# Optimization experiments

Measured on AMD Instinct MI355X. Metric: run time of the kernel, lower is better.

Reference implementation:

```python
import jax, jax.numpy as jnp
import numpy as np

N = 50000   # nodes
E = 800000  # edges
K = 3       # hops per TAGConv


def _row_normalize(x):
    row_sum = jnp.clip(jnp.sum(x, axis=1, keepdims=True), 1e-8, None)
    return x / row_sum


def _gcn_norm(edge_index, num_nodes):
    # PyG gcn_norm with add_self_loops=False (TAGConv default), edge_weight=1
    src, dst = edge_index[0], edge_index[1]
    deg = jax.ops.segment_sum(jnp.ones((src.shape[0],), jnp.float32), dst,
                              num_segments=num_nodes)
    deg_inv_sqrt = jnp.where(deg > 0, jnp.where(deg > 0, deg, 1.0) ** -0.5, 0.0)
    return deg_inv_sqrt[src] * deg_inv_sqrt[dst]  # [E]


def _propagate(x, src, dst, norm, num_nodes):
    # out[dst] += norm * x[src]   (sparse sym-normalized SpMM)
    return jax.ops.segment_sum(norm[:, None] * x[src], dst, num_segments=num_nodes)


def _tagconv(x, edge_index, norm, W, b):
    # W: [K+1, d_in, d_out]; out = sum_k A_hat^k x @ W_k + b
    src, dst = edge_index[0], edge_index[1]
    n = x.shape[0]
    hops = [x]
    for _ in range(W.shape[0] - 1):
        hops.append(_propagate(hops[-1], src, dst, norm, n))
    H = jnp.stack(hops)  # [K+1, N, d_in]
    return jnp.einsum('knd,kdo->no', H, W) + b


def setup_inputs() -> dict:
    key = jax.random.key(0)
    k1, k2, k3, k4 = jax.random.split(key, 4)
    x = jax.random.normal(k1, (N, 128), jnp.float32)
    edge_index = jax.random.randint(k2, (2, E), 0, N, jnp.int32)
    W1 = jax.random.normal(k3, (K + 1, 128, 16), jnp.float32) * 0.1
    b1 = jnp.zeros((16,), jnp.float32)
    W2 = jax.random.normal(k4, (K + 1, 16, 64), jnp.float32) * 0.1
    b2 = jnp.zeros((64,), jnp.float32)
    return {"x": x, "edge_index": edge_index, "W1": W1, "b1": b1,
            "W2": W2, "b2": b2}


def reference(x, edge_index, W1, b1, W2, b2):
    n = x.shape[0]
    norm = _gcn_norm(edge_index, n)
    h = _row_normalize(x)
    h = jax.nn.relu(_tagconv(h, edge_index, norm, W1, b1))
    # dropout is identity in eval mode
    return _tagconv(h, edge_index, norm, W2, b2)
```

## Files before the change

kernel.cpp:

```cpp
#include <hip/hip_runtime.h>
#include <hip/hip_bf16.h>

typedef unsigned short u16;

__device__ __forceinline__ float bf2f(u16 h) {
    return __uint_as_float(((unsigned int)h) << 16);
}
__device__ __forceinline__ u16 f2bf(float f) {
    __hip_bfloat16 h = __float2bfloat16(f);
    return *reinterpret_cast<u16*>(&h);
}

#define BKT_SHIFT 7
#define BKT_SIZE  128
#define CHUNK     2048

__global__ __launch_bounds__(256) void hist_kernel(const int* __restrict__ dst,
                                                   int* __restrict__ hist,
                                                   int E, int nbA, int nbuck) {
    __shared__ int lh[512];
    for (int j = threadIdx.x; j < nbuck; j += 256) lh[j] = 0;
    __syncthreads();
    int base = blockIdx.x * CHUNK;
    int end  = min(E, base + CHUNK);
    for (int e = base + threadIdx.x; e < end; e += 256)
        atomicAdd(&lh[dst[e] >> BKT_SHIFT], 1);
    __syncthreads();
    for (int j = threadIdx.x; j < nbuck; j += 256)
        hist[j * nbA + blockIdx.x] = lh[j];
}

__global__ __launch_bounds__(256) void scanA_kernel(const int* __restrict__ in,
                                                    int* __restrict__ outp1,
                                                    int* __restrict__ bsum, int n) {
    __shared__ int lds[256];
    int i = blockIdx.x * 256 + threadIdx.x;
    int v = (i < n) ? in[i] : 0;
    lds[threadIdx.x] = v;
    __syncthreads();
    #pragma unroll
    for (int off = 1; off < 256; off <<= 1) {
        int t = (threadIdx.x >= off) ? lds[threadIdx.x - off] : 0;
        __syncthreads();
        lds[threadIdx.x] += t;
        __syncthreads();
    }
    if (i < n) outp1[i + 1] = lds[threadIdx.x];
    if (threadIdx.x == 255) bsum[blockIdx.x] = lds[255];
}
__global__ __launch_bounds__(1024) void scanB_kernel(int* __restrict__ bsum, int nb) {
    __shared__ int lds[1024];
    int t = threadIdx.x;
    int v = (t < nb) ? bsum[t] : 0;
    lds[t] = v;
    __syncthreads();
    #pragma unroll
    for (int off = 1; off < 1024; off <<= 1) {
        int u = (t >= off) ? lds[t - off] : 0;
        __syncthreads();
        lds[t] += u;
        __syncthreads();
    }
    if (t < nb) bsum[t] = lds[t] - v;
}
__global__ __launch_bounds__(256) void scanC_kernel(int* __restrict__ outp1,
                                                    const int* __restrict__ bsum, int n) {
    int i = blockIdx.x * 256 + threadIdx.x;
    if (i < n) outp1[i + 1] += bsum[blockIdx.x];
    if (i == 0) outp1[0] = 0;
}

__global__ __launch_bounds__(256) void bucket_scatter_kernel(
    const int* __restrict__ src, const int* __restrict__ dst,
    const int* __restrict__ hofs, int2* __restrict__ bucketed,
    int E, int nbA, int nbuck)
{
    __shared__ int lbase[512];
    __shared__ int lcnt[512];
    for (int j = threadIdx.x; j < nbuck; j += 256) {
        lbase[j] = hofs[j * nbA + blockIdx.x];
        lcnt[j] = 0;
    }
    __syncthreads();
    int base = blockIdx.x * CHUNK;
    int end  = min(E, base + CHUNK);
    for (int e = base + threadIdx.x; e < end; e += 256) {
        int d = dst[e];
        int b = d >> BKT_SHIFT;
        int r = atomicAdd(&lcnt[b], 1);
        bucketed[lbase[b] + r] = make_int2(src[e], d);
    }
}

__global__ __launch_bounds__(256) void csr_finalize_kernel(
    const int2* __restrict__ bucketed, const int* __restrict__ hofs,
    int* __restrict__ rowptr, float* __restrict__ dis,
    float2* __restrict__ ecolw, int E, int nbA, int nbuck, int n)
{
    __shared__ int cnt[BKT_SIZE];
    __shared__ int run[BKT_SIZE];
    __shared__ float disl[BKT_SIZE];
    int b = blockIdx.x;
    int bstart = hofs[b * nbA];
    int bend   = (b == nbuck - 1) ? E : hofs[(b + 1) * nbA];
    for (int j = threadIdx.x; j < BKT_SIZE; j += 256) cnt[j] = 0;
    __syncthreads();
    for (int i = bstart + threadIdx.x; i < bend; i += 256)
        atomicAdd(&cnt[bucketed[i].y & (BKT_SIZE - 1)], 1);
    __syncthreads();
    if (threadIdx.x == 0) {
        int runacc = 0;
        for (int j = 0; j < BKT_SIZE; ++j) {
            int c = cnt[j];
            run[j] = runacc;
            runacc += c;
        }
    }
    __syncthreads();
    for (int j = threadIdx.x; j < BKT_SIZE; j += 256) {
        int d = b * BKT_SIZE + j;
        if (d < n) {
            rowptr[d] = bstart + run[j];
            int c = cnt[j];
            float dv = (c > 0) ? rsqrtf((float)c) : 0.0f;
            dis[d] = dv;
            disl[j] = dv;
        }
    }
    if (b == 0 && threadIdx.x == 0) rowptr[n] = E;
    __syncthreads();
    for (int i = bstart + threadIdx.x; i < bend; i += 256) {
        int2 p = bucketed[i];
        int j = p.y & (BKT_SIZE - 1);
        int r = atomicAdd(&run[j], 1);
        ecolw[bstart + r] = make_float2(__int_as_float(p.x), disl[j]);
    }
}

__global__ __launch_bounds__(256) void weight_kernel(float2* __restrict__ ecolw,
                                                     const float* __restrict__ dis, int E) {
    int e = blockIdx.x * blockDim.x + threadIdx.x;
    if (e < E) {
        float2 c = ecolw[e];
        ecolw[e].y = c.y * dis[__float_as_int(c.x)];
    }
}

__global__ __launch_bounds__(256) void gemm1_bf_kernel(
    const float* __restrict__ x, const float* __restrict__ W1,
    u16* __restrict__ zb, int n, int nstride)
{
    __shared__ float As[64 * 132];
    __shared__ float Bs[64 * 64];
    __shared__ float sums[128];
    const int t  = threadIdx.x;
    const int tx = t & 15;
    const int ty = t >> 4;
    const int c  = t & 15;
    const int g  = t >> 4;
    const int block_row = blockIdx.x * 128;

    float acc[8][4];
    #pragma unroll
    for (int i = 0; i < 8; ++i)
        #pragma unroll
        for (int j = 0; j < 4; ++j) acc[i][j] = 0.f;

    for (int kp = 0; kp < 2; ++kp) {
        #pragma unroll
        for (int i = 0; i < 8; ++i) {
            int row  = g + 16 * i;
            int grow = block_row + row;
            float v0 = 0.f, v1 = 0.f, v2 = 0.f, v3 = 0.f;
            if (grow < n) {
                const float* xp = x + (long)grow * 128 + kp * 64 + c;
                v0 = xp[0]; v1 = xp[16]; v2 = xp[32]; v3 = xp[48];
            }
            As[(c +  0) * 132 + row] = v0;
            As[(c + 16) * 132 + row] = v1;
            As[(c + 32) * 132 + row] = v2;
            As[(c + 48) * 132 + row] = v3;
            float red = (v0 + v1) + (v2 + v3);
            #pragma unroll
            for (int off = 8; off > 0; off >>= 1) red += __shfl_down(red, off, 16);
            if (c == 0) { if (kp == 0) sums[row] = red; else sums[row] += red; }
        }
        #pragma unroll
        for (int i2 = 0; i2 < 4; ++i2) {
            int kk = g + 16 * i2;
            int kglob = kp * 64 + kk;
            float4 wv = *(const float4*)(W1 + (c >> 2) * 2048 + kglob * 16 + 4 * (c & 3));
            *(float4*)(Bs + kk * 64 + 4 * c) = wv;
        }
        __syncthreads();
        #pragma unroll 4
        for (int kk = 0; kk < 64; ++kk) {
            float4 a0 = *(const float4*)(As + kk * 132 + 8 * ty);
            float4 a1 = *(const float4*)(As + kk * 132 + 8 * ty + 4);
            float4 bv = *(const float4*)(Bs + kk * 64 + 4 * tx);
            float ar[8] = {a0.x, a0.y, a0.z, a0.w, a1.x, a1.y, a1.z, a1.w};
            float br[4] = {bv.x, bv.y, bv.z, bv.w};
            #pragma unroll
            for (int i = 0; i < 8; ++i)
                #pragma unroll
                for (int j = 0; j < 4; ++j)
                    acc[i][j] += ar[i] * br[j];
        }
        __syncthreads();
    }
    int plane = tx >> 2;
    int oo4   = 4 * (tx & 3);
    #pragma unroll
    for (int i = 0; i < 8; ++i) {
        int row  = 8 * ty + i;
        int grow = block_row + row;
        if (grow < n) {
            float s = 1.0f / fmaxf(sums[row], 1e-8f);
            ushort4 o;
            o.x = f2bf(acc[i][0] * s); o.y = f2bf(acc[i][1] * s);
            o.z = f2bf(acc[i][2] * s); o.w = f2bf(acc[i][3] * s);
            *(ushort4*)(zb + (long)plane * nstride + (long)grow * 16 + oo4) = o;
        }
    }
}

__global__ __launch_bounds__(256) void spmm_csr_bf_kernel(
    const u16* __restrict__ in, const u16* __restrict__ addsrc,
    u16* __restrict__ out, const int* __restrict__ rowptr,
    const float2* __restrict__ ecolw, const float* __restrict__ b,
    int relu, int n)
{
    int t = blockIdx.x * blockDim.x + threadIdx.x;
    int r = t >> 2, q = t & 3;
    if (r >= n) return;
    int e0 = rowptr[r], e1 = rowptr[r + 1];
    float a0x=0,a0y=0,a0z=0,a0w=0, a1x=0,a1y=0,a1z=0,a1w=0;
    float a2x=0,a2y=0,a2z=0,a2w=0, a3x=0,a3y=0,a3z=0,a3w=0;
    int e = e0;
    for (; e + 4 <= e1; e += 4) {
        float2 c0 = ecolw[e], c1 = ecolw[e+1], c2 = ecolw[e+2], c3 = ecolw[e+3];
        ushort4 v0 = *((const ushort4*)(in + (long)__float_as_int(c0.x) * 16) + q);
        ushort4 v1 = *((const ushort4*)(in + (long)__float_as_int(c1.x) * 16) + q);
        ushort4 v2 = *((const ushort4*)(in + (long)__float_as_int(c2.x) * 16) + q);
        ushort4 v3 = *((const ushort4*)(in + (long)__float_as_int(c3.x) * 16) + q);
        a0x += c0.y * bf2f(v0.x); a0y += c0.y * bf2f(v0.y); a0z += c0.y * bf2f(v0.z); a0w += c0.y * bf2f(v0.w);
        a1x += c1.y * bf2f(v1.x); a1y += c1.y * bf2f(v1.y); a1z += c1.y * bf2f(v1.z); a1w += c1.y * bf2f(v1.w);
        a2x += c2.y * bf2f(v2.x); a2y += c2.y * bf2f(v2.y); a2z += c2.y * bf2f(v2.z); a2w += c2.y * bf2f(v2.w);
        a3x += c3.y * bf2f(v3.x); a3y += c3.y * bf2f(v3.y); a3z += c3.y * bf2f(v3.z); a3w += c3.y * bf2f(v3.w);
    }
    for (; e < e1; ++e) {
        float2 c0 = ecolw[e];
        ushort4 v0 = *((const ushort4*)(in + (long)__float_as_int(c0.x) * 16) + q);
        a0x += c0.y * bf2f(v0.x); a0y += c0.y * bf2f(v0.y); a0z += c0.y * bf2f(v0.z); a0w += c0.y * bf2f(v0.w);
    }
    float Ax = (a0x+a1x)+(a2x+a3x), Ay = (a0y+a1y)+(a2y+a3y);
    float Az = (a0z+a1z)+(a2z+a3z), Aw = (a0w+a1w)+(a2w+a3w);
    if (addsrc) {
        ushort4 s = *((const ushort4*)(addsrc + (long)r * 16) + q);
        Ax += bf2f(s.x); Ay += bf2f(s.y); Az += bf2f(s.z); Aw += bf2f(s.w);
    }
    if (b) {
        float4 bb = *((const float4*)b + q);
        Ax += bb.x; Ay += bb.y; Az += bb.z; Aw += bb.w;
    }
    if (relu) {
        Ax = fmaxf(Ax, 0.f); Ay = fmaxf(Ay, 0.f);
        Az = fmaxf(Az, 0.f); Aw = fmaxf(Aw, 0.f);
    }
    ushort4 o; o.x = f2bf(Ax); o.y = f2bf(Ay); o.z = f2bf(Az); o.w = f2bf(Aw);
    *((ushort4*)(out + (long)r * 16) + q) = o;
}

__global__ __launch_bounds__(256) void gemm2_bf_kernel(
    const u16* __restrict__ zb, const float* __restrict__ W2,
    const float* __restrict__ b2, float* __restrict__ out, int n, int nstride)
{
    __shared__ float As[64 * 132];
    __shared__ float Bs[64 * 64];
    const int t  = threadIdx.x;
    const int tx = t & 15;
    const int ty = t >> 4;
    const int c  = t & 15;
    const int g  = t >> 4;
    const int block_row = blockIdx.x * 128;

    float acc[8][4];
    #pragma unroll
    for (int i = 0; i < 8; ++i)
        #pragma unroll
        for (int j = 0; j < 4; ++j) acc[i][j] = 0.f;

    #pragma unroll
    for (int i = 0; i < 8; ++i) {
        int row  = g + 16 * i;
        int grow = block_row + row;
        float v0 = 0.f, v1 = 0.f, v2 = 0.f, v3 = 0.f;
        if (grow < n) {
            const u16* zp = zb + (long)grow * 16 + c;
            v0 = bf2f(zp[0]);
            v1 = bf2f(zp[(long)nstride]);
            v2 = bf2f(zp[2 * (long)nstride]);
            v3 = bf2f(zp[3 * (long)nstride]);
        }
        As[(c +  0) * 132 + row] = v0;
        As[(c + 16) * 132 + row] = v1;
        As[(c + 32) * 132 + row] = v2;
        As[(c + 48) * 132 + row] = v3;
    }
    #pragma unroll
    for (int i2 = 0; i2 < 4; ++i2) {
        int j = g + 16 * i2;
        float4 wv = *(const float4*)(W2 + j * 64 + 4 * c);
        *(float4*)(Bs + j * 64 + 4 * c) = wv;
    }
    __syncthreads();
    #pragma unroll 4
    for (int kk = 0; kk < 64; ++kk) {
        float4 a0 = *(const float4*)(As + kk * 132 + 8 * ty);
        float4 a1 = *(const float4*)(As + kk * 132 + 8 * ty + 4);
        float4 bv = *(const float4*)(Bs + kk * 64 + 4 * tx);
        float ar[8] = {a0.x, a0.y, a0.z, a0.w, a1.x, a1.y, a1.z, a1.w};
        float br[4] = {bv.x, bv.y, bv.z, bv.w};
        #pragma unroll
        for (int i = 0; i < 8; ++i)
            #pragma unroll
            for (int j = 0; j < 4; ++j)
                acc[i][j] += ar[i] * br[j];
    }
    float4 bias = *(const float4*)(b2 + 4 * tx);
    #pragma unroll
    for (int i = 0; i < 8; ++i) {
        int grow = block_row + 8 * ty + i;
        if (grow < n) {
            float4 o = make_float4(acc[i][0] + bias.x, acc[i][1] + bias.y,
                                   acc[i][2] + bias.z, acc[i][3] + bias.w);
            *(float4*)(out + (long)grow * 64 + 4 * tx) = o;
        }
    }
}

__global__ void deg_kernel(const int* __restrict__ dst, float* __restrict__ deg, int E) {
    int e = blockIdx.x * blockDim.x + threadIdx.x;
    if (e < E) atomicAdd(&deg[dst[e]], 1.0f);
}
__global__ void disf_kernel(float* __restrict__ deg, int n) {
    int i = blockIdx.x * blockDim.x + threadIdx.x;
    if (i < n) {
        float d = deg[i];
        deg[i] = (d > 0.0f) ? rsqrtf(d) : 0.0f;
    }
}
__global__ __launch_bounds__(256) void gemm1_f32_kernel(
    const float* __restrict__ x, const float* __restrict__ W1,
    float* __restrict__ z, int n, int nstride)
{
    __shared__ float As[64 * 132];
    __shared__ float Bs[64 * 64];
    __shared__ float sums[128];
    const int t  = threadIdx.x;
    const int tx = t & 15;
    const int ty = t >> 4;
    const int c  = t & 15;
    const int g  = t >> 4;
    const int block_row = blockIdx.x * 128;
    float acc[8][4];
    #pragma unroll
    for (int i = 0; i < 8; ++i)
        #pragma unroll
        for (int j = 0; j < 4; ++j) acc[i][j] = 0.f;
    for (int kp = 0; kp < 2; ++kp) {
        #pragma unroll
        for (int i = 0; i < 8; ++i) {
            int row  = g + 16 * i;
            int grow = block_row + row;
            float v0 = 0.f, v1 = 0.f, v2 = 0.f, v3 = 0.f;
            if (grow < n) {
                const float* xp = x + (long)grow * 128 + kp * 64 + c;
                v0 = xp[0]; v1 = xp[16]; v2 = xp[32]; v3 = xp[48];
            }
            As[(c +  0) * 132 + row] = v0;
            As[(c + 16) * 132 + row] = v1;
            As[(c + 32) * 132 + row] = v2;
            As[(c + 48) * 132 + row] = v3;
            float red = (v0 + v1) + (v2 + v3);
            #pragma unroll
            for (int off = 8; off > 0; off >>= 1) red += __shfl_down(red, off, 16);
            if (c == 0) { if (kp == 0) sums[row] = red; else sums[row] += red; }
        }
        #pragma unroll
        for (int i2 = 0; i2 < 4; ++i2) {
            int kk = g + 16 * i2;
            int kglob = kp * 64 + kk;
            float4 wv = *(const float4*)(W1 + (c >> 2) * 2048 + kglob * 16 + 4 * (c & 3));
            *(float4*)(Bs + kk * 64 + 4 * c) = wv;
        }
        __syncthreads();
        #pragma unroll 4
        for (int kk = 0; kk < 64; ++kk) {
            float4 a0 = *(const float4*)(As + kk * 132 + 8 * ty);
            float4 a1 = *(const float4*)(As + kk * 132 + 8 * ty + 4);
            float4 bv = *(const float4*)(Bs + kk * 64 + 4 * tx);
            float ar[8] = {a0.x, a0.y, a0.z, a0.w, a1.x, a1.y, a1.z, a1.w};
            float br[4] = {bv.x, bv.y, bv.z, bv.w};
            #pragma unroll
            for (int i = 0; i < 8; ++i)
                #pragma unroll
                for (int j = 0; j < 4; ++j)
                    acc[i][j] += ar[i] * br[j];
        }
        __syncthreads();
    }
    int plane = tx >> 2;
    int oo4   = 4 * (tx & 3);
    #pragma unroll
    for (int i = 0; i < 8; ++i) {
        int row  = 8 * ty + i;
        int grow = block_row + row;
        if (grow < n) {
            float s = 1.0f / fmaxf(sums[row], 1e-8f);
            float4 o = make_float4(acc[i][0] * s, acc[i][1] * s, acc[i][2] * s, acc[i][3] * s);
            *(float4*)(z + (long)plane * nstride + (long)grow * 16 + oo4) = o;
        }
    }
}
__global__ __launch_bounds__(256) void spmm_atomic_kernel(
    const float* __restrict__ in, float* __restrict__ out,
    const int* __restrict__ src, const int* __restrict__ dst,
    const float* __restrict__ dis, int E)
{
    int t = blockIdx.x * blockDim.x + threadIdx.x;
    int e = t >> 4, f = t & 15;
    if (e < E) {
        int s = src[e], d = dst[e];
        atomicAdd(&out[d * 16 + f], dis[s] * dis[d] * in[s * 16 + f]);
    }
}
__global__ void bias_relu_kernel(float* __restrict__ z0, const float* __restrict__ b, int total) {
    int i = blockIdx.x * blockDim.x + threadIdx.x;
    if (i < total) {
        float v = z0[i] + b[i & 15];
        z0[i] = v > 0.0f ? v : 0.0f;
    }
}
__global__ __launch_bounds__(256) void gemm2_f32_kernel(
    const float* __restrict__ z, const float* __restrict__ W2,
    const float* __restrict__ b2, float* __restrict__ out, int n, int nstride)
{
    __shared__ float As[64 * 132];
    __shared__ float Bs[64 * 64];
    const int t  = threadIdx.x;
    const int tx = t & 15;
    const int ty = t >> 4;
    const int c  = t & 15;
    const int g  = t >> 4;
    const int block_row = blockIdx.x * 128;
    float acc[8][4];
    #pragma unroll
    for (int i = 0; i < 8; ++i)
        #pragma unroll
        for (int j = 0; j < 4; ++j) acc[i][j] = 0.f;
    #pragma unroll
    for (int i = 0; i < 8; ++i) {
        int row  = g + 16 * i;
        int grow = block_row + row;
        float v0 = 0.f, v1 = 0.f, v2 = 0.f, v3 = 0.f;
        if (grow < n) {
            const float* zp = z + (long)grow * 16 + c;
            v0 = zp[0];
            v1 = zp[(long)nstride];
            v2 = zp[2 * (long)nstride];
            v3 = zp[3 * (long)nstride];
        }
        As[(c +  0) * 132 + row] = v0;
        As[(c + 16) * 132 + row] = v1;
        As[(c + 32) * 132 + row] = v2;
        As[(c + 48) * 132 + row] = v3;
    }
    #pragma unroll
    for (int i2 = 0; i2 < 4; ++i2) {
        int j = g + 16 * i2;
        float4 wv = *(const float4*)(W2 + j * 64 + 4 * c);
        *(float4*)(Bs + j * 64 + 4 * c) = wv;
    }
    __syncthreads();
    #pragma unroll 4
    for (int kk = 0; kk < 64; ++kk) {
        float4 a0 = *(const float4*)(As + kk * 132 + 8 * ty);
        float4 a1 = *(const float4*)(As + kk * 132 + 8 * ty + 4);
        float4 bv = *(const float4*)(Bs + kk * 64 + 4 * tx);
        float ar[8] = {a0.x, a0.y, a0.z, a0.w, a1.x, a1.y, a1.z, a1.w};
        float br[4] = {bv.x, bv.y, bv.z, bv.w};
        #pragma unroll
        for (int i = 0; i < 8; ++i)
            #pragma unroll
            for (int j = 0; j < 4; ++j)
                acc[i][j] += ar[i] * br[j];
    }
    float4 bias = *(const float4*)(b2 + 4 * tx);
    #pragma unroll
    for (int i = 0; i < 8; ++i) {
        int grow = block_row + 8 * ty + i;
        if (grow < n) {
            float4 o = make_float4(acc[i][0] + bias.x, acc[i][1] + bias.y,
                                   acc[i][2] + bias.z, acc[i][3] + bias.w);
            *(float4*)(out + (long)grow * 64 + 4 * tx) = o;
        }
    }
}

static inline size_t align16(size_t v) { return (v + 15) & ~(size_t)15; }

extern "C" void kernel_launch(void* const* d_in, const int* in_sizes, int n_in,
                              void* d_out, int out_size, void* d_ws, size_t ws_size,
                              hipStream_t stream) {
    const float* x   = (const float*)d_in[0];
    const int*   ei  = (const int*)d_in[1];
    const float* W1  = (const float*)d_in[2];
    const float* b1  = (const float*)d_in[3];
    const float* W2  = (const float*)d_in[4];
    const float* bb2 = (const float*)d_in[5];
    float* out = (float*)d_out;

    const int n  = in_sizes[0] / 128;
    const int E  = in_sizes[1] / 2;
    const int NS = n * 16;

    const int* srcp = ei;
    const int* dstp = ei + E;

    const int nbuck = (n + BKT_SIZE - 1) >> BKT_SHIFT;
    const int nbA   = (E + CHUNK - 1) / CHUNK;
    const int m     = nbuck * nbA;
    const int nbS   = (m + 255) / 256;

    char* wsb = (char*)d_ws;
    int*   hist   = (int*)wsb;
    int*   hofs   = (int*)(wsb + (size_t)4 * m);
    int*   bsum   = (int*)(wsb + (size_t)4 * (2 * m + 1));
    int*   rowptr = (int*)(wsb + (size_t)4 * (2 * m + 1 + 1024));
    float* dis    = (float*)(wsb + (size_t)4 * (2 * m + 1 + 1024 + n + 1));
    size_t zoffb  = align16((size_t)4 * (2 * m + 1 + 1024 + 2 * n + 1));
    u16*   zb     = (u16*)(wsb + zoffb);
    size_t bkoff  = align16(zoffb + (size_t)2 * 4 * NS);
    int2*  bucketed = (int2*)(wsb + bkoff);
    size_t ecooff = align16(bkoff + (size_t)8 * E);
    float2* ecolw = (float2*)(wsb + ecooff);
    size_t need   = ecooff + (size_t)8 * E;

    int gemm_blocks = (n + 127) / 128;

    if (ws_size >= need && nbuck <= 512 && nbS <= 256 * 1024) {
        hist_kernel<<<nbA, 256, 0, stream>>>(dstp, hist, E, nbA, nbuck);
        if (nbS <= 1024) {
            scanA_kernel<<<nbS, 256, 0, stream>>>(hist, hofs, bsum, m);
            scanB_kernel<<<1, 1024, 0, stream>>>(bsum, nbS);
            scanC_kernel<<<nbS, 256, 0, stream>>>(hofs, bsum, m);
        }
        bucket_scatter_kernel<<<nbA, 256, 0, stream>>>(srcp, dstp, hofs, bucketed, E, nbA, nbuck);
        csr_finalize_kernel<<<nbuck, 256, 0, stream>>>(bucketed, hofs, rowptr, dis, ecolw, E, nbA, nbuck, n);
        weight_kernel<<<(E + 255) / 256, 256, 0, stream>>>(ecolw, dis, E);

        gemm1_bf_kernel<<<gemm_blocks, 256, 0, stream>>>(x, W1, zb, n, NS);

        int sb = (4 * n + 255) / 256;
        spmm_csr_bf_kernel<<<sb, 256, 0, stream>>>(zb + 3 * NS, zb + 2 * NS, zb + 2 * NS, rowptr, ecolw, nullptr, 0, n);
        spmm_csr_bf_kernel<<<sb, 256, 0, stream>>>(zb + 2 * NS, zb + 1 * NS, zb + 1 * NS, rowptr, ecolw, nullptr, 0, n);
        spmm_csr_bf_kernel<<<sb, 256, 0, stream>>>(zb + 1 * NS, zb,          zb,          rowptr, ecolw, b1,      1, n);
        spmm_csr_bf_kernel<<<sb, 256, 0, stream>>>(zb,          nullptr, zb + 1 * NS, rowptr, ecolw, nullptr, 0, n);
        spmm_csr_bf_kernel<<<sb, 256, 0, stream>>>(zb + 1 * NS, nullptr, zb + 2 * NS, rowptr, ecolw, nullptr, 0, n);
        spmm_csr_bf_kernel<<<sb, 256, 0, stream>>>(zb + 2 * NS, nullptr, zb + 3 * NS, rowptr, ecolw, nullptr, 0, n);

        gemm2_bf_kernel<<<gemm_blocks, 256, 0, stream>>>(zb, W2, bb2, out, n, NS);
    } else {
        float* ws = (float*)d_ws;
        float* dis2 = ws;
        size_t z2off = ((size_t)n + 3) & ~(size_t)3;
        float* z2 = ws + z2off;
        hipMemsetAsync(dis2, 0, n * sizeof(float), stream);
        deg_kernel<<<(E + 255) / 256, 256, 0, stream>>>(dstp, dis2, E);
        disf_kernel<<<(n + 255) / 256, 256, 0, stream>>>(dis2, n);
        gemm1_f32_kernel<<<gemm_blocks, 256, 0, stream>>>(x, W1, z2, n, NS);
        int sb = (16 * E + 255) / 256;
        spmm_atomic_kernel<<<sb, 256, 0, stream>>>(z2 + 3 * NS, z2 + 2 * NS, srcp, dstp, dis2, E);
        spmm_atomic_kernel<<<sb, 256, 0, stream>>>(z2 + 2 * NS, z2 + 1 * NS, srcp, dstp, dis2, E);
        spmm_atomic_kernel<<<sb, 256, 0, stream>>>(z2 + 1 * NS, z2,          srcp, dstp, dis2, E);
        bias_relu_kernel<<<(NS + 255) / 256, 256, 0, stream>>>(z2, b1, NS);
        hipMemsetAsync(z2 + NS, 0, (size_t)3 * NS * sizeof(float), stream);
        spmm_atomic_kernel<<<sb, 256, 0, stream>>>(z2,          z2 + NS,     srcp, dstp, dis2, E);
        spmm_atomic_kernel<<<sb, 256, 0, stream>>>(z2 + NS,     z2 + 2 * NS, srcp, dstp, dis2, E);
        spmm_atomic_kernel<<<sb, 256, 0, stream>>>(z2 + 2 * NS, z2 + 3 * NS, srcp, dstp, dis2, E);
        gemm2_f32_kernel<<<gemm_blocks, 256, 0, stream>>>(z2, W2, bb2, out, n, NS);
    }
}
```

Baseline: 214.7 us.

## Replace CSR build with bucketed edges and LDS-atomic bucket SpMM

Drops the per-row CSR finalize pass. Edges are now packed into 32-bit words holding the source and the local row, bucketed by 64-row destination groups. Degrees come from a per-bucket count, and each SpMM block accumulates its 64 rows in shared memory with LDS atomics, applying the destination normalization at write-out. This removes the finalize sort and the rowptr reads, but adds shared-memory atomic contention in every SpMM and makes the float summation order nondeterministic.

Result: slower. 672.2 us (+213.1%).

```diff
diff --git a/kernel.cpp b/kernel.cpp
--- a/kernel.cpp
+++ b/kernel.cpp
@@ -2,23 +2,24 @@
 #include <hip/hip_bf16.h>
 
 typedef unsigned short u16;
+typedef unsigned int u32;
 
 __device__ __forceinline__ float bf2f(u16 h) {
-    return __uint_as_float(((unsigned int)h) << 16);
+    return __uint_as_float(((u32)h) << 16);
 }
 __device__ __forceinline__ u16 f2bf(float f) {
     __hip_bfloat16 h = __float2bfloat16(f);
     return *reinterpret_cast<u16*>(&h);
 }
 
-#define BKT_SHIFT 7
-#define BKT_SIZE  128
-#define CHUNK     2048
+#define BKT_SHIFT 6
+#define BKT_SIZE  64
+#define CHUNK     4096
 
 __global__ __launch_bounds__(256) void hist_kernel(const int* __restrict__ dst,
                                                    int* __restrict__ hist,
                                                    int E, int nbA, int nbuck) {
-    __shared__ int lh[512];
+    __shared__ int lh[1024];
     for (int j = threadIdx.x; j < nbuck; j += 256) lh[j] = 0;
     __syncthreads();
     int base = blockIdx.x * CHUNK;
@@ -72,11 +73,11 @@
 
 __global__ __launch_bounds__(256) void bucket_scatter_kernel(
     const int* __restrict__ src, const int* __restrict__ dst,
-    const int* __restrict__ hofs, int2* __restrict__ bucketed,
+    const int* __restrict__ hofs, u32* __restrict__ bucketed,
     int E, int nbA, int nbuck)
 {
-    __shared__ int lbase[512];
-    __shared__ int lcnt[512];
+    __shared__ int lbase[1024];
+    __shared__ int lcnt[1024];
     for (int j = threadIdx.x; j < nbuck; j += 256) {
         lbase[j] = hofs[j * nbA + blockIdx.x];
         lcnt[j] = 0;
@@ -88,61 +89,110 @@
         int d = dst[e];
         int b = d >> BKT_SHIFT;
         int r = atomicAdd(&lcnt[b], 1);
-        bucketed[lbase[b] + r] = make_int2(src[e], d);
-    }
-}
-
-__global__ __launch_bounds__(256) void csr_finalize_kernel(
-    const int2* __restrict__ bucketed, const int* __restrict__ hofs,
-    int* __restrict__ rowptr, float* __restrict__ dis,
-    float2* __restrict__ ecolw, int E, int nbA, int nbuck, int n)
+        bucketed[lbase[b] + r] = (u32)src[e] | ((u32)(d & (BKT_SIZE - 1)) << 20);
+    }
+}
+
+__global__ __launch_bounds__(256) void bucketdeg_kernel(
+    const u32* __restrict__ bucketed, const int* __restrict__ hofs,
+    float* __restrict__ dis, int E, int nbA, int nbuck, int n)
 {
     __shared__ int cnt[BKT_SIZE];
-    __shared__ int run[BKT_SIZE];
-    __shared__ float disl[BKT_SIZE];
-    int b = blockIdx.x;
-    int bstart = hofs[b * nbA];
-    int bend   = (b == nbuck - 1) ? E : hofs[(b + 1) * nbA];
-    for (int j = threadIdx.x; j < BKT_SIZE; j += 256) cnt[j] = 0;
-    __syncthreads();
-    for (int i = bstart + threadIdx.x; i < bend; i += 256)
-        atomicAdd(&cnt[bucketed[i].y & (BKT_SIZE - 1)], 1);
-    __syncthreads();
-    if (threadIdx.x == 0) {
-        int runacc = 0;
-        for (int j = 0; j < BKT_SIZE; ++j) {
-            int c = cnt[j];
-            run[j] = runacc;
-            runacc += c;
-        }
-    }
-    __syncthreads();
-    for (int j = threadIdx.x; j < BKT_SIZE; j += 256) {
-        int d = b * BKT_SIZE + j;
-        if (d < n) {
-            rowptr[d] = bstart + run[j];
-            int c = cnt[j];
-            float dv = (c > 0) ? rsqrtf((float)c) : 0.0f;
-            dis[d] = dv;
-            disl[j] = dv;
-        }
-    }
-    if (b == 0 && threadIdx.x == 0) rowptr[n] = E;
-    __syncthreads();
-    for (int i = bstart + threadIdx.x; i < bend; i += 256) {
-        int2 p = bucketed[i];
-        int j = p.y & (BKT_SIZE - 1);
-        int r = atomicAdd(&run[j], 1);
-        ecolw[bstart + r] = make_float2(__int_as_float(p.x), disl[j]);
-    }
-}
-
-__global__ __launch_bounds__(256) void weight_kernel(float2* __restrict__ ecolw,
-                                                     const float* __restrict__ dis, int E) {
+    int bkt = blockIdx.x;
+    if (threadIdx.x < BKT_SIZE) cnt[threadIdx.x] = 0;
+    __syncthreads();
+    int estart = hofs[bkt * nbA];
+    int eend   = (bkt + 1 < nbuck) ? hofs[(bkt + 1) * nbA] : E;
+    for (int e = estart + threadIdx.x; e < eend; e += 256)
+        atomicAdd(&cnt[bucketed[e] >> 20], 1);
+    __syncthreads();
+    if (threadIdx.x < BKT_SIZE) {
+        int r = bkt * BKT_SIZE + threadIdx.x;
+        if (r < n) {
+            int c = cnt[threadIdx.x];
+            dis[r] = (c > 0) ? rsqrtf((float)c) : 0.0f;
+        }
+    }
+}
+
+__global__ __launch_bounds__(256) void weight_kernel(const u32* __restrict__ bucketed,
+                                                     const float* __restrict__ dis,
+                                                     float2* __restrict__ ecolw, int E) {
     int e = blockIdx.x * blockDim.x + threadIdx.x;
     if (e < E) {
-        float2 c = ecolw[e];
-        ecolw[e].y = c.y * dis[__float_as_int(c.x)];
+        u32 p = bucketed[e];
+        ecolw[e] = make_float2(__int_as_float((int)p), dis[p & 0xFFFFFu]);
+    }
+}
+
+__global__ __launch_bounds__(256) void spmm_bucket_kernel(
+    const u16* __restrict__ in, const u16* __restrict__ addsrc,
+    u16* __restrict__ out, const int* __restrict__ hofs,
+    const float2* __restrict__ ecolw, const float* __restrict__ dis,
+    const float* __restrict__ b, int relu, int E, int nbA, int nbuck, int n)
+{
+    __shared__ float acc[BKT_SIZE * 16];
+    int bkt = blockIdx.x;
+    int estart = hofs[bkt * nbA];
+    int eend   = (bkt + 1 < nbuck) ? hofs[(bkt + 1) * nbA] : E;
+    #pragma unroll
+    for (int j = threadIdx.x; j < BKT_SIZE * 16; j += 256) acc[j] = 0.f;
+    __syncthreads();
+
+    int g = threadIdx.x >> 2;
+    int q = threadIdx.x & 3;
+    int e = estart + g;
+    for (; e + 64 < eend; e += 128) {
+        float2 c0 = ecolw[e];
+        float2 c1 = ecolw[e + 64];
+        u32 p0 = (u32)__float_as_int(c0.x);
+        u32 p1 = (u32)__float_as_int(c1.x);
+        ushort4 v0 = *((const ushort4*)(in + (size_t)(p0 & 0xFFFFFu) * 16) + q);
+        ushort4 v1 = *((const ushort4*)(in + (size_t)(p1 & 0xFFFFFu) * 16) + q);
+        float* a0 = acc + (p0 >> 20) * 16 + 4 * q;
+        float* a1 = acc + (p1 >> 20) * 16 + 4 * q;
+        atomicAdd(a0 + 0, c0.y * bf2f(v0.x));
+        atomicAdd(a0 + 1, c0.y * bf2f(v0.y));
+        atomicAdd(a0 + 2, c0.y * bf2f(v0.z));
+        atomicAdd(a0 + 3, c0.y * bf2f(v0.w));
+        atomicAdd(a1 + 0, c1.y * bf2f(v1.x));
+        atomicAdd(a1 + 1, c1.y * bf2f(v1.y));
+        atomicAdd(a1 + 2, c1.y * bf2f(v1.z));
+        atomicAdd(a1 + 3, c1.y * bf2f(v1.w));
+    }
+    if (e < eend) {
+        float2 c0 = ecolw[e];
+        u32 p0 = (u32)__float_as_int(c0.x);
+        ushort4 v0 = *((const ushort4*)(in + (size_t)(p0 & 0xFFFFFu) * 16) + q);
+        float* a0 = acc + (p0 >> 20) * 16 + 4 * q;
+        atomicAdd(a0 + 0, c0.y * bf2f(v0.x));
+        atomicAdd(a0 + 1, c0.y * bf2f(v0.y));
+        atomicAdd(a0 + 2, c0.y * bf2f(v0.z));
+        atomicAdd(a0 + 3, c0.y * bf2f(v0.w));
+    }
+    __syncthreads();
+
+    int row = threadIdx.x >> 2;
+    int qq  = threadIdx.x & 3;
+    int r   = bkt * BKT_SIZE + row;
+    if (r < n) {
+        float dr = dis[r];
+        const float* ap = acc + row * 16 + 4 * qq;
+        float Ax = ap[0] * dr, Ay = ap[1] * dr, Az = ap[2] * dr, Aw = ap[3] * dr;
+        if (addsrc) {
+            ushort4 s = *((const ushort4*)(addsrc + (size_t)r * 16) + qq);
+            Ax += bf2f(s.x); Ay += bf2f(s.y); Az += bf2f(s.z); Aw += bf2f(s.w);
+        }
+        if (b) {
+            float4 bb = *((const float4*)b + qq);
+            Ax += bb.x; Ay += bb.y; Az += bb.z; Aw += bb.w;
+        }
+        if (relu) {
+            Ax = fmaxf(Ax, 0.f); Ay = fmaxf(Ay, 0.f);
+            Az = fmaxf(Az, 0.f); Aw = fmaxf(Aw, 0.f);
+        }
+        ushort4 o; o.x = f2bf(Ax); o.y = f2bf(Ay); o.z = f2bf(Az); o.w = f2bf(Aw);
+        *((ushort4*)(out + (size_t)r * 16) + qq) = o;
     }
 }
 
@@ -224,53 +274,6 @@
     }
 }
 
-__global__ __launch_bounds__(256) void spmm_csr_bf_kernel(
-    const u16* __restrict__ in, const u16* __restrict__ addsrc,
-    u16* __restrict__ out, const int* __restrict__ rowptr,
-    const float2* __restrict__ ecolw, const float* __restrict__ b,
-    int relu, int n)
-{
-    int t = blockIdx.x * blockDim.x + threadIdx.x;
-    int r = t >> 2, q = t & 3;
-    if (r >= n) return;
-    int e0 = rowptr[r], e1 = rowptr[r + 1];
-    float a0x=0,a0y=0,a0z=0,a0w=0, a1x=0,a1y=0,a1z=0,a1w=0;
-    float a2x=0,a2y=0,a2z=0,a2w=0, a3x=0,a3y=0,a3z=0,a3w=0;
-    int e = e0;
-    for (; e + 4 <= e1; e += 4) {
-        float2 c0 = ecolw[e], c1 = ecolw[e+1], c2 = ecolw[e+2], c3 = ecolw[e+3];
-        ushort4 v0 = *((const ushort4*)(in + (long)__float_as_int(c0.x) * 16) + q);
-        ushort4 v1 = *((const ushort4*)(in + (long)__float_as_int(c1.x) * 16) + q);
-        ushort4 v2 = *((const ushort4*)(in + (long)__float_as_int(c2.x) * 16) + q);
-        ushort4 v3 = *((const ushort4*)(in + (long)__float_as_int(c3.x) * 16) + q);
-        a0x += c0.y * bf2f(v0.x); a0y += c0.y * bf2f(v0.y); a0z += c0.y * bf2f(v0.z); a0w += c0.y * bf2f(v0.w);
-        a1x += c1.y * bf2f(v1.x); a1y += c1.y * bf2f(v1.y); a1z += c1.y * bf2f(v1.z); a1w += c1.y * bf2f(v1.w);
-        a2x += c2.y * bf2f(v2.x); a2y += c2.y * bf2f(v2.y); a2z += c2.y * bf2f(v2.z); a2w += c2.y * bf2f(v2.w);
-        a3x += c3.y * bf2f(v3.x); a3y += c3.y * bf2f(v3.y); a3z += c3.y * bf2f(v3.z); a3w += c3.y * bf2f(v3.w);
-    }
-    for (; e < e1; ++e) {
-        float2 c0 = ecolw[e];
-        ushort4 v0 = *((const ushort4*)(in + (long)__float_as_int(c0.x) * 16) + q);
-        a0x += c0.y * bf2f(v0.x); a0y += c0.y * bf2f(v0.y); a0z += c0.y * bf2f(v0.z); a0w += c0.y * bf2f(v0.w);
-    }
-    float Ax = (a0x+a1x)+(a2x+a3x), Ay = (a0y+a1y)+(a2y+a3y);
-    float Az = (a0z+a1z)+(a2z+a3z), Aw = (a0w+a1w)+(a2w+a3w);
-    if (addsrc) {
-        ushort4 s = *((const ushort4*)(addsrc + (long)r * 16) + q);
-        Ax += bf2f(s.x); Ay += bf2f(s.y); Az += bf2f(s.z); Aw += bf2f(s.w);
-    }
-    if (b) {
-        float4 bb = *((const float4*)b + q);
-        Ax += bb.x; Ay += bb.y; Az += bb.z; Aw += bb.w;
-    }
-    if (relu) {
-        Ax = fmaxf(Ax, 0.f); Ay = fmaxf(Ay, 0.f);
-        Az = fmaxf(Az, 0.f); Aw = fmaxf(Aw, 0.f);
-    }
-    ushort4 o; o.x = f2bf(Ax); o.y = f2bf(Ay); o.z = f2bf(Az); o.w = f2bf(Aw);
-    *((ushort4*)(out + (long)r * 16) + q) = o;
-}
-
 __global__ __launch_bounds__(256) void gemm2_bf_kernel(
     const u16* __restrict__ zb, const float* __restrict__ W2,
     const float* __restrict__ b2, float* __restrict__ out, int n, int nstride)
@@ -537,38 +540,34 @@
     int*   hist   = (int*)wsb;
     int*   hofs   = (int*)(wsb + (size_t)4 * m);
     int*   bsum   = (int*)(wsb + (size_t)4 * (2 * m + 1));
-    int*   rowptr = (int*)(wsb + (size_t)4 * (2 * m + 1 + 1024));
-    float* dis    = (float*)(wsb + (size_t)4 * (2 * m + 1 + 1024 + n + 1));
-    size_t zoffb  = align16((size_t)4 * (2 * m + 1 + 1024 + 2 * n + 1));
+    float* dis    = (float*)(wsb + (size_t)4 * (2 * m + 1 + 1024));
+    size_t zoffb  = align16((size_t)4 * (2 * m + 1 + 1024 + n));
     u16*   zb     = (u16*)(wsb + zoffb);
     size_t bkoff  = align16(zoffb + (size_t)2 * 4 * NS);
-    int2*  bucketed = (int2*)(wsb + bkoff);
-    size_t ecooff = align16(bkoff + (size_t)8 * E);
+    u32*   bucketed = (u32*)(wsb + bkoff);
+    size_t ecooff = align16(bkoff + (size_t)4 * E);
     float2* ecolw = (float2*)(wsb + ecooff);
     size_t need   = ecooff + (size_t)8 * E;
 
     int gemm_blocks = (n + 127) / 128;
 
-    if (ws_size >= need && nbuck <= 512 && nbS <= 256 * 1024) {
+    if (ws_size >= need && n < (1 << 20) && nbuck <= 1024 && nbS <= 1024) {
         hist_kernel<<<nbA, 256, 0, stream>>>(dstp, hist, E, nbA, nbuck);
-        if (nbS <= 1024) {
-            scanA_kernel<<<nbS, 256, 0, stream>>>(hist, hofs, bsum, m);
-            scanB_kernel<<<1, 1024, 0, stream>>>(bsum, nbS);
-            scanC_kernel<<<nbS, 256, 0, stream>>>(hofs, bsum, m);
-        }
+        scanA_kernel<<<nbS, 256, 0, stream>>>(hist, hofs, bsum, m);
+        scanB_kernel<<<1, 1024, 0, stream>>>(bsum, nbS);
+        scanC_kernel<<<nbS, 256, 0, stream>>>(hofs, bsum, m);
         bucket_scatter_kernel<<<nbA, 256, 0, stream>>>(srcp, dstp, hofs, bucketed, E, nbA, nbuck);
-        csr_finalize_kernel<<<nbuck, 256, 0, stream>>>(bucketed, hofs, rowptr, dis, ecolw, E, nbA, nbuck, n);
-        weight_kernel<<<(E + 255) / 256, 256, 0, stream>>>(ecolw, dis, E);
+        bucketdeg_kernel<<<nbuck, 256, 0, stream>>>(bucketed, hofs, dis, E, nbA, nbuck, n);
+        weight_kernel<<<(E + 255) / 256, 256, 0, stream>>>(bucketed, dis, ecolw, E);
 
         gemm1_bf_kernel<<<gemm_blocks, 256, 0, stream>>>(x, W1, zb, n, NS);
 
-        int sb = (4 * n + 255) / 256;
-        spmm_csr_bf_kernel<<<sb, 256, 0, stream>>>(zb + 3 * NS, zb + 2 * NS, zb + 2 * NS, rowptr, ecolw, nullptr, 0, n);
-        spmm_csr_bf_kernel<<<sb, 256, 0, stream>>>(zb + 2 * NS, zb + 1 * NS, zb + 1 * NS, rowptr, ecolw, nullptr, 0, n);
-        spmm_csr_bf_kernel<<<sb, 256, 0, stream>>>(zb + 1 * NS, zb,          zb,          rowptr, ecolw, b1,      1, n);
-        spmm_csr_bf_kernel<<<sb, 256, 0, stream>>>(zb,          nullptr, zb + 1 * NS, rowptr, ecolw, nullptr, 0, n);
-        spmm_csr_bf_kernel<<<sb, 256, 0, stream>>>(zb + 1 * NS, nullptr, zb + 2 * NS, rowptr, ecolw, nullptr, 0, n);
-        spmm_csr_bf_kernel<<<sb, 256, 0, stream>>>(zb + 2 * NS, nullptr, zb + 3 * NS, rowptr, ecolw, nullptr, 0, n);
+        spmm_bucket_kernel<<<nbuck, 256, 0, stream>>>(zb + 3 * NS, zb + 2 * NS, zb + 2 * NS, hofs, ecolw, dis, nullptr, 0, E, nbA, nbuck, n);
+        spmm_bucket_kernel<<<nbuck, 256, 0, stream>>>(zb + 2 * NS, zb + 1 * NS, zb + 1 * NS, hofs, ecolw, dis, nullptr, 0, E, nbA, nbuck, n);
+        spmm_bucket_kernel<<<nbuck, 256, 0, stream>>>(zb + 1 * NS, zb,          zb,          hofs, ecolw, dis, b1,      1, E, nbA, nbuck, n);
+        spmm_bucket_kernel<<<nbuck, 256, 0, stream>>>(zb,          nullptr, zb + 1 * NS, hofs, ecolw, dis, nullptr, 0, E, nbA, nbuck, n);
+        spmm_bucket_kernel<<<nbuck, 256, 0, stream>>>(zb + 1 * NS, nullptr, zb + 2 * NS, hofs, ecolw, dis, nullptr, 0, E, nbA, nbuck, n);
+        spmm_bucket_kernel<<<nbuck, 256, 0, stream>>>(zb + 2 * NS, nullptr, zb + 3 * NS, hofs, ecolw, dis, nullptr, 0, E, nbA, nbuck, n);
 
         gemm2_bf_kernel<<<gemm_blocks, 256, 0, stream>>>(zb, W2, bb2, out, n, NS);
     } else {
```
